# Optimization experiments

Measured on AMD Instinct MI355X. Metric: run time of the kernel, lower is better.

The kernel has to match this reference:

```python
import jax, jax.numpy as jnp
import numpy as np

C_IN = 256
C_RED = max(4, C_IN // 4)  # 64


def setup_inputs() -> dict:
    key = jax.random.key(0)
    k1, k2, k3, k4, k5 = jax.random.split(key, 5)
    B, C, H, W = 4, C_IN, 64, 64
    x = jax.random.normal(k1, (B, C, H, W), dtype=jnp.float32)
    # 1x1 convs (no bias) are just channel matmuls: weight shape (out_ch, in_ch)
    s_in = 1.0 / np.sqrt(C)
    s_red = 1.0 / np.sqrt(C_RED)
    Wq = jax.random.normal(k2, (C_RED, C), dtype=jnp.float32) * s_in
    Wk = jax.random.normal(k3, (C_RED, C), dtype=jnp.float32) * s_in
    Wv = jax.random.normal(k4, (C_RED, C), dtype=jnp.float32) * s_in
    Wp = jax.random.normal(k5, (C, C_RED), dtype=jnp.float32) * s_red
    return {"x": x, "Wq": Wq, "Wk": Wk, "Wv": Wv, "Wp": Wp}


def reference(x, Wq, Wk, Wv, Wp):
    B, C, H, W = x.shape
    N = H * W
    xf = x.reshape(B, C, N)                       # (B, C, N)
    q = jnp.einsum('rc,bcn->bnr', Wq, xf)         # (B, N, c_red)
    k = jnp.einsum('rc,bcn->brn', Wk, xf)         # (B, c_red, N)
    v = jnp.einsum('rc,bcn->bnr', Wv, xf)         # (B, N, c_red)
    scale = 1.0 / jnp.sqrt(jnp.float32(k.shape[1]))
    attn = jnp.einsum('bnr,brm->bnm', q, k) * scale   # (B, N, N)
    attn = jax.nn.softmax(attn, axis=-1)
    out = jnp.einsum('bnm,bmr->brn', attn, v)     # (B, c_red, N)
    out = jnp.einsum('cr,brn->bcn', Wp, out)      # (B, C, N)
    return out.reshape(B, C, H, W) + x
```

## Files before the change

### kernel.cpp

```cpp
#include <hip/hip_runtime.h>
#include <hip/hip_bf16.h>

#define CIN 256
#define CRED 64
#define NB 4
#define NN 4096

typedef float v4f __attribute__((ext_vector_type(4)));
typedef short v8s __attribute__((ext_vector_type(8)));
typedef unsigned short u16;
typedef u16 u16x4 __attribute__((ext_vector_type(4)));
typedef u16 u16x8 __attribute__((ext_vector_type(8)));
typedef unsigned int u32;

#define LOG2E 1.4426950408889634f

__device__ __forceinline__ u16 f2bf(float f) {
    union { float f; u32 u; } v; v.f = f;
    u32 r = (v.u + 0x7FFFu + ((v.u >> 16) & 1u)) >> 16;
    return (u16)r;
}
__device__ __forceinline__ float bf2f(u16 s) {
    union { u32 u; float f; } v; v.u = ((u32)s) << 16;
    return v.f;
}
__device__ __forceinline__ u32 pkbf(float a, float b) {
    float2 f; f.x = a; f.y = b;
    __hip_bfloat162 h = __float22bfloat162_rn(f);
    union { __hip_bfloat162 h; u32 u; } c; c.h = h;
    return c.u;
}
__device__ __forceinline__ v4f mfma16(v8s a, v8s b, v4f c) {
    return __builtin_amdgcn_mfma_f32_16x16x32_bf16(a, b, c, 0, 0, 0);
}
__device__ __forceinline__ float fexp2(float x) {
#if __has_builtin(__builtin_amdgcn_exp2f)
    return __builtin_amdgcn_exp2f(x);
#else
    return exp2f(x);
#endif
}

__global__ __launch_bounds__(256) void k_wconv(const float* __restrict__ Wq,
                                               const float* __restrict__ Wk,
                                               const float* __restrict__ Wv,
                                               u16* __restrict__ Wb) {
    int t = threadIdx.x;
    int idx = (blockIdx.x * 256 + t) * 4;
    int row = idx >> 8;
    int mat = row >> 6, r = row & 63, col = idx & 255;
    const float* src = (mat == 0) ? Wq : (mat == 1) ? Wk : Wv;
    float4 v = *(const float4*)&src[r * 256 + col];
    float s = (mat == 0) ? (0.125f * LOG2E) : 1.0f;
    u16x4 o;
    o[0] = f2bf(v.x * s); o[1] = f2bf(v.y * s);
    o[2] = f2bf(v.z * s); o[3] = f2bf(v.w * s);
    *(u16x4*)&Wb[idx] = o;
}

__global__ __launch_bounds__(256) void k_qkvm(const float* __restrict__ x,
                                              const u16* __restrict__ Wb,
                                              u16* __restrict__ Q, u16* __restrict__ K,
                                              u16* __restrict__ V) {
    __shared__ __align__(16) u16 Xl[1056 * 8];
    int t = threadIdx.x;
    int wv = t >> 6, lane = t & 63, c15 = lane & 15, quad = lane >> 4;
    int n0g = blockIdx.x * 32;
    int b = n0g >> 12, nb = n0g & 4095;
    const float* xb = x + ((size_t)b << 20);

    {
        int cb = t >> 3, n4 = (t & 7) * 4;
        const float* px = xb + (size_t)(cb * 8) * 4096 + nb + n4;
        float4 f[8];
#pragma unroll
        for (int j = 0; j < 8; ++j)
            f[j] = *(const float4*)&px[(size_t)j * 4096];
#pragma unroll
        for (int i = 0; i < 4; ++i) {
            union { u16x8 v; u32 w[4]; } pk;
            pk.w[0] = pkbf(((const float*)&f[0])[i], ((const float*)&f[1])[i]);
            pk.w[1] = pkbf(((const float*)&f[2])[i], ((const float*)&f[3])[i]);
            pk.w[2] = pkbf(((const float*)&f[4])[i], ((const float*)&f[5])[i]);
            pk.w[3] = pkbf(((const float*)&f[6])[i], ((const float*)&f[7])[i]);
            *(u16x8*)&Xl[(size_t)(cb * 33 + n4 + i) * 8] = pk.v;
        }
    }
    __syncthreads();

    v8s Af[2][8];
#pragma unroll
    for (int nt = 0; nt < 2; ++nt)
#pragma unroll
        for (int kc = 0; kc < 8; ++kc)
            Af[nt][kc] = *(const v8s*)&Xl[(size_t)((kc * 4 + quad) * 33 + nt * 16 + c15) * 8];

#pragma unroll
    for (int rti = 0; rti < 3; ++rti) {
        int rt = wv * 3 + rti;
        const u16* wrow = Wb + (size_t)(rt * 16 + c15) * 256 + quad * 8;
        v8s Bf[8];
#pragma unroll
        for (int kc = 0; kc < 8; ++kc) Bf[kc] = *(const v8s*)&wrow[kc * 32];
#pragma unroll
        for (int nt = 0; nt < 2; ++nt) {
            v4f acc = {0.f, 0.f, 0.f, 0.f};
#pragma unroll
            for (int kc = 0; kc < 8; ++kc)
                acc = mfma16(Af[nt][kc], Bf[kc], acc);
            if (rt < 8) {
                u16* base = (rt < 4) ? Q : K;
                u16* dst = base + ((size_t)b << 18)
                         + (size_t)(nb + nt * 16 + quad * 4) * 64
                         + (rt & 3) * 16 + c15;
#pragma unroll
                for (int g = 0; g < 4; ++g) dst[g * 64] = f2bf(acc[g]);
            } else {
                int hi2 = ((nb + nt * 16) >> 4) & 3;
                size_t base = ((size_t)b * 64 + (rt - 8) * 16 + c15) * 4096
                            + (size_t)((nb + nt * 16) & ~63)
                            + (hi2 >> 1) * 32 + (hi2 & 1) * 4 + quad * 8;
                union { u16x4 v; u32 w[2]; } pv;
                pv.w[0] = pkbf(acc[0], acc[1]);
                pv.w[1] = pkbf(acc[2], acc[3]);
                *(u16x4*)&V[base] = pv.v;
            }
        }
    }
}

__global__ __launch_bounds__(256, 2) void k_flash(const u16* __restrict__ Q,
                                                  const u16* __restrict__ K,
                                                  const u16* __restrict__ V,
                                                  u16* __restrict__ OP,
                                                  float* __restrict__ Lb,
                                                  int sh) {
    __shared__ __align__(16) u16 KV[2][2][4096];
    int t = threadIdx.x;
    int p = blockIdx.x & ((1u << sh) - 1);
    int tile = blockIdx.x >> sh;
    int b = tile >> 5;
    int n0 = (tile & 31) * 128;
    int wv = t >> 6;
    int lane = t & 63;
    int c15 = lane & 15;
    int quad = lane >> 4;
    int nw = n0 + wv * 32;
    const u16* Qb = Q + ((size_t)b << 18);
    const u16* Kb = K + ((size_t)b << 18);
    const u16* Vb = V + ((size_t)b << 18);

    v8s Qa[2][2];
#pragma unroll
    for (int rg = 0; rg < 2; ++rg)
#pragma unroll
        for (int c2 = 0; c2 < 2; ++c2)
            Qa[rg][c2] = *(const v8s*)&Qb[(size_t)(nw + rg * 16 + c15) * 64 + c2 * 32 + quad * 8];

    union { u16x8 u; v8s s; } on;
#pragma unroll
    for (int j = 0; j < 8; ++j) on.u[j] = 0x3F80;

    v4f O[2][4];
    v4f Lacc[2];
#pragma unroll
    for (int rg = 0; rg < 2; ++rg) {
#pragma unroll
        for (int g = 0; g < 4; ++g) {
            Lacc[rg][g] = 0.f;
#pragma unroll
            for (int cg = 0; cg < 4; ++cg) O[rg][cg][g] = 0.f;
        }
    }

    int mlen = NN >> sh;
    int m0 = p * mlen;
    int iters = mlen >> 6;

    int lrow = lane >> 3;
    int cs16 = (((lane & 7) ^ lrow) << 3);
    const u16* gK = Kb + ((size_t)(wv * 16 + lrow) << 6) + cs16;
    const u16* gV = Vb + ((size_t)(wv * 16 + lrow) << 12) + cs16;

    auto stage = [&](int buf, int mt) {
#pragma unroll
        for (int i = 0; i < 2; ++i) {
            __builtin_amdgcn_global_load_lds(
                (const __attribute__((address_space(1))) void*)(gK + ((size_t)(mt + i * 8) << 6)),
                (__attribute__((address_space(3))) void*)&KV[buf][0][(wv * 2 + i) << 9],
                16, 0, 0);
            __builtin_amdgcn_global_load_lds(
                (const __attribute__((address_space(1))) void*)(gV + ((size_t)i << 15) + mt),
                (__attribute__((address_space(3))) void*)&KV[buf][1][(wv * 2 + i) << 9],
                16, 0, 0);
        }
    };

    int swz = (c15 & 7) << 4;
    int col0 = (quad << 4) ^ swz;
    int col1 = col0 ^ 64;
    int rbase = c15 << 7;

    stage(0, m0);
    __syncthreads();

    for (int it = 0; it < iters; ++it) {
        int cur = it & 1;
        if (it + 1 < iters) stage(cur ^ 1, m0 + (it + 1) * 64);
        const char* KB = (const char*)&KV[cur][0][0];
        const char* VB = (const char*)&KV[cur][1][0];

        v4f S[2][4];
#pragma unroll
        for (int rg = 0; rg < 2; ++rg)
#pragma unroll
            for (int s = 0; s < 4; ++s)
#pragma unroll
                for (int g = 0; g < 4; ++g) S[rg][s][g] = 0.f;

        __builtin_amdgcn_s_setprio(1);
#pragma unroll
        for (int s = 0; s < 4; ++s) {
            v8s kb0 = *(const v8s*)(KB + rbase + s * 2048 + col0);
            v8s kb1 = *(const v8s*)(KB + rbase + s * 2048 + col1);
            S[0][s] = mfma16(kb0, Qa[0][0], S[0][s]);
            S[1][s] = mfma16(kb0, Qa[1][0], S[1][s]);
            S[0][s] = mfma16(kb1, Qa[0][1], S[0][s]);
            S[1][s] = mfma16(kb1, Qa[1][1], S[1][s]);
        }
        __builtin_amdgcn_s_setprio(0);

        v8s Pa[2][2];
#pragma unroll
        for (int rg = 0; rg < 2; ++rg)
#pragma unroll
            for (int c2 = 0; c2 < 2; ++c2) {
                int s0 = c2 * 2, s1 = c2 * 2 + 1;
                union { v8s s; u32 w[4]; } pk;
                pk.w[0] = pkbf(fexp2(S[rg][s0][0]), fexp2(S[rg][s0][1]));
                pk.w[1] = pkbf(fexp2(S[rg][s0][2]), fexp2(S[rg][s0][3]));
                pk.w[2] = pkbf(fexp2(S[rg][s1][0]), fexp2(S[rg][s1][1]));
                pk.w[3] = pkbf(fexp2(S[rg][s1][2]), fexp2(S[rg][s1][3]));
                Pa[rg][c2] = pk.s;
            }

        __builtin_amdgcn_s_setprio(1);
#pragma unroll
        for (int cg = 0; cg < 4; ++cg) {
            v8s vb0 = *(const v8s*)(VB + (cg << 11) + rbase + col0);
            v8s vb1 = *(const v8s*)(VB + (cg << 11) + rbase + col1);
            O[0][cg] = mfma16(Pa[0][0], vb0, O[0][cg]);
            O[1][cg] = mfma16(Pa[1][0], vb0, O[1][cg]);
            O[0][cg] = mfma16(Pa[0][1], vb1, O[0][cg]);
            O[1][cg] = mfma16(Pa[1][1], vb1, O[1][cg]);
        }
        Lacc[0] = mfma16(Pa[0][0], on.s, Lacc[0]);
        Lacc[0] = mfma16(Pa[0][1], on.s, Lacc[0]);
        Lacc[1] = mfma16(Pa[1][0], on.s, Lacc[1]);
        Lacc[1] = mfma16(Pa[1][1], on.s, Lacc[1]);
        __builtin_amdgcn_s_setprio(0);
        __syncthreads();
    }

    u16* OPp = OP + (size_t)p * (NB * NN * 64) + (size_t)b * NN * 64;
#pragma unroll
    for (int rg = 0; rg < 2; ++rg)
#pragma unroll
        for (int cg = 0; cg < 4; ++cg)
#pragma unroll
            for (int g = 0; g < 4; ++g) {
                int n = nw + rg * 16 + quad * 4 + g;
                OPp[(size_t)n * 64 + cg * 16 + c15] = f2bf(O[rg][cg][g]);
            }
    if (c15 == 0) {
        float* Lp = Lb + (size_t)p * (NB * NN) + (size_t)b * NN;
#pragma unroll
        for (int rg = 0; rg < 2; ++rg)
#pragma unroll
            for (int g = 0; g < 4; ++g) {
                int n = nw + rg * 16 + quad * 4 + g;
                Lp[n] = Lacc[rg][g];
            }
    }
}

#define OMP 72
template <int NSP>
__global__ __launch_bounds__(256) void k_proj(const u16* __restrict__ OP,
                                              const float* __restrict__ Lb,
                                              const float* __restrict__ Wp,
                                              const float* __restrict__ x,
                                              float* __restrict__ out) {
    __shared__ __align__(16) u16 Om[32 * OMP];
    int t = threadIdx.x;
    int b = blockIdx.x >> 7;
    int n0 = (blockIdx.x & 127) * 32;

    {
        int n_l = t >> 3, r0 = (t & 7) * 8;
        size_t nidx = (size_t)b * NN + n0 + n_l;
        float o[8] = {0.f, 0.f, 0.f, 0.f, 0.f, 0.f, 0.f, 0.f};
        float l = 0.f;
#pragma unroll
        for (int p = 0; p < NSP; ++p) {
            u16x8 u = *(const u16x8*)&OP[((size_t)p * (NB * NN) + nidx) * 64 + r0];
#pragma unroll
            for (int j = 0; j < 8; ++j) o[j] += bf2f(u[j]);
            l += Lb[(size_t)p * (NB * NN) + nidx];
        }
        float inv = 1.0f / l;
        union { u16x8 v; u32 w[4]; } p2;
        p2.w[0] = pkbf(o[0] * inv, o[1] * inv);
        p2.w[1] = pkbf(o[2] * inv, o[3] * inv);
        p2.w[2] = pkbf(o[4] * inv, o[5] * inv);
        p2.w[3] = pkbf(o[6] * inv, o[7] * inv);
        *(u16x8*)&Om[n_l * OMP + r0] = p2.v;
    }
    __syncthreads();

    int lane = t & 63, wvv = t >> 6, c15 = lane & 15, quad = lane >> 4;
    v8s Bf[2][2];
#pragma unroll
    for (int nt = 0; nt < 2; ++nt) {
        Bf[nt][0] = *(const v8s*)&Om[(nt * 16 + c15) * OMP + quad * 8];
        Bf[nt][1] = *(const v8s*)&Om[(nt * 16 + c15) * OMP + 32 + quad * 8];
    }
#pragma unroll
    for (int ct0 = 0; ct0 < 4; ++ct0) {
        int ct = wvv * 4 + ct0;
        const float* wrow = Wp + (size_t)(ct * 16 + c15) * 64 + quad * 8;
        float4 wa = *(const float4*)&wrow[0];
        float4 wb = *(const float4*)&wrow[4];
        float4 wc = *(const float4*)&wrow[32];
        float4 wd = *(const float4*)&wrow[36];
        union { v8s s; u32 w[4]; } A0, A1;
        A0.w[0] = pkbf(wa.x, wa.y); A0.w[1] = pkbf(wa.z, wa.w);
        A0.w[2] = pkbf(wb.x, wb.y); A0.w[3] = pkbf(wb.z, wb.w);
        A1.w[0] = pkbf(wc.x, wc.y); A1.w[1] = pkbf(wc.z, wc.w);
        A1.w[2] = pkbf(wd.x, wd.y); A1.w[3] = pkbf(wd.z, wd.w);
#pragma unroll
        for (int nt = 0; nt < 2; ++nt) {
            v4f acc = {0.f, 0.f, 0.f, 0.f};
            acc = mfma16(A0.s, Bf[nt][0], acc);
            acc = mfma16(A1.s, Bf[nt][1], acc);
            size_t base = ((size_t)(b * 256 + ct * 16 + quad * 4)) * 4096 + n0 + nt * 16 + c15;
#pragma unroll
            for (int g = 0; g < 4; ++g)
                out[base + (size_t)g * 4096] = acc[g] + x[base + (size_t)g * 4096];
        }
    }
}

extern "C" void kernel_launch(void* const* d_in, const int* in_sizes, int n_in,
                              void* d_out, int out_size, void* d_ws, size_t ws_size,
                              hipStream_t stream) {
    const float* x  = (const float*)d_in[0];
    const float* Wq = (const float*)d_in[1];
    const float* Wk = (const float*)d_in[2];
    const float* Wv = (const float*)d_in[3];
    const float* Wp = (const float*)d_in[4];
    float* out = (float*)d_out;
    char* ws = (char*)d_ws;

    const int nsp = 4;
    const int sh = 2;

    u16* Wb  = (u16*)(ws);
    u16* Q   = (u16*)(ws + 262144);
    u16* K   = (u16*)(ws + 262144 + 2097152);
    u16* V   = (u16*)(ws + 262144 + 2 * 2097152);
    u16* OP  = (u16*)(ws + 262144 + 3 * 2097152);
    float* Lbuf = (float*)(ws + 262144 + (size_t)(3 + nsp) * 2097152);

    k_wconv<<<48, 256, 0, stream>>>(Wq, Wk, Wv, Wb);
    k_qkvm<<<512, 256, 0, stream>>>(x, Wb, Q, K, V);
    k_flash<<<NB * 32 * nsp, 256, 0, stream>>>(Q, K, V, OP, Lbuf, sh);
    k_proj<4><<<NB * 128, 256, 0, stream>>>(OP, Lbuf, Wp, x, out);
}
```

Baseline: 114.4 us.

## Split flash tile across waves by key halves with 64-row query groups

Reorganises the four waves of the attention block into two query halves of 64 rows each and two key halves of 32 keys per tile. Each wave now reuses every K/V fragment it reads from LDS across four query row groups, roughly halving LDS reads per MFMA. The cost is an in-block reduction at the end, where partial O and row sums go through shared memory. The wave holding the second key half then sits idle during the final write, and register pressure grows from the doubled O, Lacc and Q fragments.

```diff
diff --git a/kernel.cpp b/kernel.cpp
--- a/kernel.cpp
+++ b/kernel.cpp
@@ -136,6 +136,7 @@
                                                   float* __restrict__ Lb,
                                                   int sh) {
     __shared__ __align__(16) u16 KV[2][2][4096];
+    __shared__ __align__(16) v4f LshV[2][4][64];
     int t = threadIdx.x;
     int p = blockIdx.x & ((1u << sh) - 1);
     int tile = blockIdx.x >> sh;
@@ -145,14 +146,15 @@
     int lane = t & 63;
     int c15 = lane & 15;
     int quad = lane >> 4;
-    int nw = n0 + wv * 32;
+    int qh = wv >> 1, kh = wv & 1;
+    int nw = n0 + qh * 64;
     const u16* Qb = Q + ((size_t)b << 18);
     const u16* Kb = K + ((size_t)b << 18);
     const u16* Vb = V + ((size_t)b << 18);
 
-    v8s Qa[2][2];
-#pragma unroll
-    for (int rg = 0; rg < 2; ++rg)
+    v8s Qa[4][2];
+#pragma unroll
+    for (int rg = 0; rg < 4; ++rg)
 #pragma unroll
         for (int c2 = 0; c2 < 2; ++c2)
             Qa[rg][c2] = *(const v8s*)&Qb[(size_t)(nw + rg * 16 + c15) * 64 + c2 * 32 + quad * 8];
@@ -161,10 +163,10 @@
 #pragma unroll
     for (int j = 0; j < 8; ++j) on.u[j] = 0x3F80;
 
-    v4f O[2][4];
-    v4f Lacc[2];
-#pragma unroll
-    for (int rg = 0; rg < 2; ++rg) {
+    v4f O[4][4];
+    v4f Lacc[4];
+#pragma unroll
+    for (int rg = 0; rg < 4; ++rg) {
 #pragma unroll
         for (int g = 0; g < 4; ++g) {
             Lacc[rg][g] = 0.f;
@@ -197,9 +199,11 @@
     };
 
     int swz = (c15 & 7) << 4;
-    int col0 = (quad << 4) ^ swz;
-    int col1 = col0 ^ 64;
-    int rbase = c15 << 7;
+    int colK0 = (quad << 4) ^ swz;
+    int colK1 = colK0 ^ 64;
+    int colV  = ((kh << 6) | (quad << 4)) ^ swz;
+    int rbaseK = kh * 4096 + (c15 << 7);
+    int rbaseV = c15 << 7;
 
     stage(0, m0);
     __syncthreads();
@@ -210,77 +214,99 @@
         const char* KB = (const char*)&KV[cur][0][0];
         const char* VB = (const char*)&KV[cur][1][0];
 
-        v4f S[2][4];
-#pragma unroll
-        for (int rg = 0; rg < 2; ++rg)
-#pragma unroll
-            for (int s = 0; s < 4; ++s)
+        v4f S[4][2];
+#pragma unroll
+        for (int rg = 0; rg < 4; ++rg)
+#pragma unroll
+            for (int s = 0; s < 2; ++s)
 #pragma unroll
                 for (int g = 0; g < 4; ++g) S[rg][s][g] = 0.f;
 
         __builtin_amdgcn_s_setprio(1);
 #pragma unroll
-        for (int s = 0; s < 4; ++s) {
-            v8s kb0 = *(const v8s*)(KB + rbase + s * 2048 + col0);
-            v8s kb1 = *(const v8s*)(KB + rbase + s * 2048 + col1);
-            S[0][s] = mfma16(kb0, Qa[0][0], S[0][s]);
-            S[1][s] = mfma16(kb0, Qa[1][0], S[1][s]);
-            S[0][s] = mfma16(kb1, Qa[0][1], S[0][s]);
-            S[1][s] = mfma16(kb1, Qa[1][1], S[1][s]);
+        for (int s = 0; s < 2; ++s) {
+            v8s kb0 = *(const v8s*)(KB + rbaseK + s * 2048 + colK0);
+            v8s kb1 = *(const v8s*)(KB + rbaseK + s * 2048 + colK1);
+#pragma unroll
+            for (int rg = 0; rg < 4; ++rg) {
+                S[rg][s] = mfma16(kb0, Qa[rg][0], S[rg][s]);
+                S[rg][s] = mfma16(kb1, Qa[rg][1], S[rg][s]);
+            }
         }
         __builtin_amdgcn_s_setprio(0);
 
-        v8s Pa[2][2];
-#pragma unroll
-        for (int rg = 0; rg < 2; ++rg)
-#pragma unroll
-            for (int c2 = 0; c2 < 2; ++c2) {
-                int s0 = c2 * 2, s1 = c2 * 2 + 1;
-                union { v8s s; u32 w[4]; } pk;
-                pk.w[0] = pkbf(fexp2(S[rg][s0][0]), fexp2(S[rg][s0][1]));
-                pk.w[1] = pkbf(fexp2(S[rg][s0][2]), fexp2(S[rg][s0][3]));
-                pk.w[2] = pkbf(fexp2(S[rg][s1][0]), fexp2(S[rg][s1][1]));
-                pk.w[3] = pkbf(fexp2(S[rg][s1][2]), fexp2(S[rg][s1][3]));
-                Pa[rg][c2] = pk.s;
-            }
+        v8s Pa[4];
+#pragma unroll
+        for (int rg = 0; rg < 4; ++rg) {
+            union { v8s s; u32 w[4]; } pk;
+            pk.w[0] = pkbf(fexp2(S[rg][0][0]), fexp2(S[rg][0][1]));
+            pk.w[1] = pkbf(fexp2(S[rg][0][2]), fexp2(S[rg][0][3]));
+            pk.w[2] = pkbf(fexp2(S[rg][1][0]), fexp2(S[rg][1][1]));
+            pk.w[3] = pkbf(fexp2(S[rg][1][2]), fexp2(S[rg][1][3]));
+            Pa[rg] = pk.s;
+        }
 
         __builtin_amdgcn_s_setprio(1);
 #pragma unroll
         for (int cg = 0; cg < 4; ++cg) {
-            v8s vb0 = *(const v8s*)(VB + (cg << 11) + rbase + col0);
-            v8s vb1 = *(const v8s*)(VB + (cg << 11) + rbase + col1);
-            O[0][cg] = mfma16(Pa[0][0], vb0, O[0][cg]);
-            O[1][cg] = mfma16(Pa[1][0], vb0, O[1][cg]);
-            O[0][cg] = mfma16(Pa[0][1], vb1, O[0][cg]);
-            O[1][cg] = mfma16(Pa[1][1], vb1, O[1][cg]);
-        }
-        Lacc[0] = mfma16(Pa[0][0], on.s, Lacc[0]);
-        Lacc[0] = mfma16(Pa[0][1], on.s, Lacc[0]);
-        Lacc[1] = mfma16(Pa[1][0], on.s, Lacc[1]);
-        Lacc[1] = mfma16(Pa[1][1], on.s, Lacc[1]);
+            v8s vb = *(const v8s*)(VB + (cg << 11) + rbaseV + colV);
+#pragma unroll
+            for (int rg = 0; rg < 4; ++rg)
+                O[rg][cg] = mfma16(Pa[rg], vb, O[rg][cg]);
+        }
+#pragma unroll
+        for (int rg = 0; rg < 4; ++rg)
+            Lacc[rg] = mfma16(Pa[rg], on.s, Lacc[rg]);
         __builtin_amdgcn_s_setprio(0);
         __syncthreads();
     }
 
-    u16* OPp = OP + (size_t)p * (NB * NN * 64) + (size_t)b * NN * 64;
-#pragma unroll
-    for (int rg = 0; rg < 2; ++rg)
-#pragma unroll
-        for (int cg = 0; cg < 4; ++cg)
-#pragma unroll
-            for (int g = 0; g < 4; ++g) {
-                int n = nw + rg * 16 + quad * 4 + g;
-                OPp[(size_t)n * 64 + cg * 16 + c15] = f2bf(O[rg][cg][g]);
+    float* Osh = (float*)&KV[0][0][0];
+    if (kh) {
+#pragma unroll
+        for (int rg = 0; rg < 4; ++rg)
+#pragma unroll
+            for (int cg = 0; cg < 4; ++cg)
+                *(v4f*)&Osh[(((qh * 16 + rg * 4 + cg) << 6) + lane) * 4] = O[rg][cg];
+#pragma unroll
+        for (int rg = 0; rg < 4; ++rg)
+            LshV[qh][rg][lane] = Lacc[rg];
+    }
+    __syncthreads();
+    if (!kh) {
+#pragma unroll
+        for (int rg = 0; rg < 4; ++rg) {
+#pragma unroll
+            for (int cg = 0; cg < 4; ++cg) {
+                v4f o2 = *(const v4f*)&Osh[(((qh * 16 + rg * 4 + cg) << 6) + lane) * 4];
+#pragma unroll
+                for (int g = 0; g < 4; ++g) O[rg][cg][g] += o2[g];
             }
-    if (c15 == 0) {
-        float* Lp = Lb + (size_t)p * (NB * NN) + (size_t)b * NN;
-#pragma unroll
-        for (int rg = 0; rg < 2; ++rg)
-#pragma unroll
-            for (int g = 0; g < 4; ++g) {
-                int n = nw + rg * 16 + quad * 4 + g;
-                Lp[n] = Lacc[rg][g];
-            }
+            v4f l2 = LshV[qh][rg][lane];
+#pragma unroll
+            for (int g = 0; g < 4; ++g) Lacc[rg][g] += l2[g];
+        }
+
+        u16* OPp = OP + (size_t)p * (NB * NN * 64) + (size_t)b * NN * 64;
+#pragma unroll
+        for (int rg = 0; rg < 4; ++rg)
+#pragma unroll
+            for (int cg = 0; cg < 4; ++cg)
+#pragma unroll
+                for (int g = 0; g < 4; ++g) {
+                    int n = nw + rg * 16 + quad * 4 + g;
+                    OPp[(size_t)n * 64 + cg * 16 + c15] = f2bf(O[rg][cg][g]);
+                }
+        if (c15 == 0) {
+            float* Lp = Lb + (size_t)p * (NB * NN) + (size_t)b * NN;
+#pragma unroll
+            for (int rg = 0; rg < 4; ++rg)
+#pragma unroll
+                for (int g = 0; g < 4; ++g) {
+                    int n = nw + rg * 16 + quad * 4 + g;
+                    Lp[n] = Lacc[rg][g];
+                }
+        }
     }
 }
 
```

After: 117.9 us. 1.03x slower.
